# Kernel optimization log

Measured on AMD Instinct MI355X. Metric: run time of the kernel, lower is better.

The kernel has to match this reference:

```python
import jax, jax.numpy as jnp
import numpy as np

B, N, M = 32, 4096, 32
IN_F, OUT_F, A = 256, 256, 8


def setup_inputs() -> dict:
    key = jax.random.key(0)
    k1, k2, k3, k4, k5 = jax.random.split(key, 5)
    fatoms = jax.random.normal(k1, (B, N, IN_F), dtype=jnp.float32)
    agraph = jax.random.randint(k2, (B, N, M), 0, N, dtype=jnp.int64)
    anchor_indices = jax.random.randint(k3, (B, A), 0, N, dtype=jnp.int64)
    # xavier-uniform-like init for W and a
    wlim = float(np.sqrt(6.0 / (IN_F + OUT_F)))
    alim = float(np.sqrt(6.0 / (2 * OUT_F + 1)))
    W = jax.random.uniform(k4, (IN_F, OUT_F), dtype=jnp.float32, minval=-wlim, maxval=wlim)
    a = jax.random.uniform(k5, (2 * OUT_F, 1), dtype=jnp.float32, minval=-alim, maxval=alim)
    return {"fatoms": fatoms, "agraph": agraph, "anchor_indices": anchor_indices, "W": W, "a": a}


def reference(fatoms, agraph, anchor_indices, W, a):
    # h: (B, N, F)
    h = jnp.matmul(fatoms, W)
    F_ = h.shape[-1]
    # gather anchor features: (B, A, F)
    anchor_feat = jnp.take_along_axis(h, anchor_indices[:, :, None], axis=1)
    # e = cat([h_self + h_anch, h_self - h_anch]) @ a, decomposed to avoid the
    # (B, N, A, 2F) intermediate: e = h @ (a1+a2) + h_anch @ (a1-a2)
    a1 = a[:F_, 0]
    a2 = a[F_:, 0]
    e = (h @ (a1 + a2))[:, :, None] + (anchor_feat @ (a1 - a2))[:, None, :]  # (B, N, A)
    # mask[b,n,k] = anchor_indices[b,k] in agraph[b,n,:]  (vectorized torch.isin)
    mask = (agraph[:, :, None, :] == anchor_indices[:, None, :, None]).any(axis=-1)  # (B, N, A)
    e = jnp.where(mask, e, jnp.float32(-1e9))
    attn = jax.nn.softmax(e, axis=-1)
    # weighted sum of anchor features: (B, N, F)
    return jnp.einsum('bna,baf->bnf', attn, anchor_feat)
```

## Files before the change

### kernel.cpp

```cpp
#include <hip/hip_runtime.h>

#define B_ 32
#define N_ 4096
#define M_ 32
#define F_ 256
#define A_ 8

typedef float f32x4 __attribute__((ext_vector_type(4)));
typedef int   i32x4 __attribute__((ext_vector_type(4)));

#define WS_AF 0
#define WS_E2 (B_ * A_ * F_)

__global__ __launch_bounds__(256) void anchor_kernel(const float* __restrict__ fatoms,
                                                     const int* __restrict__ anchor_idx,
                                                     const float* __restrict__ W,
                                                     const float* __restrict__ a,
                                                     float* __restrict__ ws) {
    int bk = blockIdx.x;
    int b  = bk / A_;
    int f  = threadIdx.x;
    __shared__ float xs[F_];
    __shared__ float red[F_];
    int idx = anchor_idx[bk];
    xs[f] = fatoms[((size_t)b * N_ + idx) * F_ + f];
    __syncthreads();
    float acc[4] = {0.f, 0.f, 0.f, 0.f};
    for (int i0 = 0; i0 < F_; i0 += 16) {
#pragma unroll
        for (int j = 0; j < 16; ++j)
            acc[j & 3] += xs[i0 + j] * W[(i0 + j) * F_ + f];
    }
    float accs = (acc[0] + acc[1]) + (acc[2] + acc[3]);
    ws[WS_AF + bk * F_ + f] = accs;
    red[f] = accs * (a[f] - a[f + F_]);
    __syncthreads();
    for (int s = 128; s > 0; s >>= 1) {
        if (f < s) red[f] += red[f + s];
        __syncthreads();
    }
    if (f == 0) ws[WS_E2 + bk] = red[0];
}

#define RPW 64

__global__ __launch_bounds__(64) void main_kernel(const int* __restrict__ agraph,
                                                  const int* __restrict__ anchor_idx,
                                                  const float* __restrict__ ws,
                                                  float* __restrict__ out) {
    int lane = threadIdx.x;
    const int chunks_per_batch = N_ / RPW;
    int b     = blockIdx.x / chunks_per_batch;
    int chunk = blockIdx.x % chunks_per_batch;
    int row0  = chunk * RPW;

    const i32x4* gp = (const i32x4*)(agraph + ((size_t)b * N_ + row0 + lane) * M_);
    i32x4 g[M_ / 4];
#pragma unroll
    for (int j = 0; j < M_ / 4; ++j) g[j] = gp[j];

    const float* af = ws + WS_AF + b * (A_ * F_);
    const float* e2 = ws + WS_E2 + b * A_;

    __shared__ float attn[RPW][A_];

    int   anch[A_];
    float e2r[A_];
#pragma unroll
    for (int k = 0; k < A_; ++k) {
        anch[k] = anchor_idx[b * A_ + k];
        e2r[k]  = e2[k];
    }
    float m8 = e2r[0];
#pragma unroll
    for (int k = 1; k < A_; ++k) m8 = fmaxf(m8, e2r[k]);
    float E[A_];
#pragma unroll
    for (int k = 0; k < A_; ++k) E[k] = __expf(e2r[k] - m8);

    f32x4 afr[A_];
#pragma unroll
    for (int k = 0; k < A_; ++k) afr[k] = *(const f32x4*)(af + k * F_ + lane * 4);

    {
        unsigned mk = 0;
#pragma unroll
        for (int j = 0; j < M_ / 4; ++j) {
#pragma unroll
            for (int k = 0; k < A_; ++k) {
                int hit = (g[j].x == anch[k]) | (g[j].y == anch[k]) |
                          (g[j].z == anch[k]) | (g[j].w == anch[k]);
                mk |= hit ? (1u << k) : 0u;
            }
        }
        float p[A_], s = 0.f;
#pragma unroll
        for (int k = 0; k < A_; ++k) { p[k] = (mk & (1u << k)) ? E[k] : 0.f; s += p[k]; }
        if (mk == 0) {
#pragma unroll
            for (int k = 0; k < A_; ++k) p[k] = 1.f;
            s = 8.f;
        }
        float rinv = __builtin_amdgcn_rcpf(s);
#pragma unroll
        for (int k = 0; k < A_; ++k) attn[lane][k] = p[k] * rinv;
    }
    __syncthreads();

    size_t base = ((size_t)b * N_ + row0) * F_ + lane * 4;
    for (int r0 = 0; r0 < RPW; r0 += 4) {
        f32x4 o[4];
#pragma unroll
        for (int u = 0; u < 4; ++u) {
            f32x4 pa = *(const f32x4*)&attn[r0 + u][0];
            f32x4 pb = *(const f32x4*)&attn[r0 + u][4];
            f32x4 t = pa.x * afr[0];
            t += pa.y * afr[1];
            t += pa.z * afr[2];
            t += pa.w * afr[3];
            t += pb.x * afr[4];
            t += pb.y * afr[5];
            t += pb.z * afr[6];
            t += pb.w * afr[7];
            o[u] = t;
        }
#pragma unroll
        for (int u = 0; u < 4; ++u)
            *(f32x4*)(out + base + (size_t)(r0 + u) * F_) = o[u];
    }
}

extern "C" void kernel_launch(void* const* d_in, const int* in_sizes, int n_in,
                              void* d_out, int out_size, void* d_ws, size_t ws_size,
                              hipStream_t stream) {
    const float* fatoms     = (const float*)d_in[0];
    const int*   agraph     = (const int*)d_in[1];
    const int*   anchor_idx = (const int*)d_in[2];
    const float* W          = (const float*)d_in[3];
    const float* a          = (const float*)d_in[4];
    float*       out        = (float*)d_out;
    float*       ws         = (float*)d_ws;

    hipLaunchKernelGGL(anchor_kernel, dim3(B_ * A_), dim3(256), 0, stream,
                       fatoms, anchor_idx, W, a, ws);
    hipLaunchKernelGGL(main_kernel, dim3(B_ * (N_ / RPW)), dim3(64), 0, stream,
                       agraph, anchor_idx, ws, out);
}
```

Baseline: 37.32 us.

## Split fused kernel into separate attention and output-store kernels

Splits the fused mask/softmax/store kernel into two launches when workspace allows. The first computes the attention weights per row and writes them to workspace; the second reads them back and writes the weighted anchor sums. The intent is to separate the agraph-read phase from the output-write phase so each kernel streams one kind of traffic. The cost is an extra launch plus writing and re-reading a (B,N,8) attention buffer. The old fused kernel is kept as a fallback when the workspace is too small.

```diff
diff --git a/kernel.cpp b/kernel.cpp
--- a/kernel.cpp
+++ b/kernel.cpp
@@ -11,6 +11,8 @@
 
 #define WS_AF 0
 #define WS_E2 (B_ * A_ * F_)
+#define WS_ATTN (WS_E2 + B_ * A_)
+#define WS_FLOATS_NEEDED (WS_ATTN + B_ * N_ * A_)
 
 __global__ __launch_bounds__(256) void anchor_kernel(const float* __restrict__ fatoms,
                                                      const int* __restrict__ anchor_idx,
@@ -42,17 +44,108 @@
     if (f == 0) ws[WS_E2 + bk] = red[0];
 }
 
-#define RPW 64
-
-__global__ __launch_bounds__(64) void main_kernel(const int* __restrict__ agraph,
+__global__ __launch_bounds__(64) void attn_kernel(const int* __restrict__ agraph,
                                                   const int* __restrict__ anchor_idx,
                                                   const float* __restrict__ ws,
-                                                  float* __restrict__ out) {
+                                                  float* __restrict__ attn) {
+    int lane = threadIdx.x;
+    const int chunks_per_batch = N_ / 64;
+    int b    = blockIdx.x / chunks_per_batch;
+    int row  = (blockIdx.x % chunks_per_batch) * 64 + lane;
+
+    const i32x4* gp = (const i32x4*)(agraph + ((size_t)b * N_ + row) * M_);
+    i32x4 g[M_ / 4];
+#pragma unroll
+    for (int j = 0; j < M_ / 4; ++j) g[j] = gp[j];
+
+    int   anch[A_];
+    float e2r[A_];
+#pragma unroll
+    for (int k = 0; k < A_; ++k) {
+        anch[k] = anchor_idx[b * A_ + k];
+        e2r[k]  = ws[WS_E2 + b * A_ + k];
+    }
+    float m8 = e2r[0];
+#pragma unroll
+    for (int k = 1; k < A_; ++k) m8 = fmaxf(m8, e2r[k]);
+    float E[A_];
+#pragma unroll
+    for (int k = 0; k < A_; ++k) E[k] = __expf(e2r[k] - m8);
+
+    unsigned mk = 0;
+#pragma unroll
+    for (int j = 0; j < M_ / 4; ++j) {
+#pragma unroll
+        for (int k = 0; k < A_; ++k) {
+            int hit = (g[j].x == anch[k]) | (g[j].y == anch[k]) |
+                      (g[j].z == anch[k]) | (g[j].w == anch[k]);
+            mk |= hit ? (1u << k) : 0u;
+        }
+    }
+    float p[A_], s = 0.f;
+#pragma unroll
+    for (int k = 0; k < A_; ++k) { p[k] = (mk & (1u << k)) ? E[k] : 0.f; s += p[k]; }
+    if (mk == 0) {
+#pragma unroll
+        for (int k = 0; k < A_; ++k) p[k] = 1.f;
+        s = 8.f;
+    }
+    float rinv = __builtin_amdgcn_rcpf(s);
+    f32x4 pa = {p[0] * rinv, p[1] * rinv, p[2] * rinv, p[3] * rinv};
+    f32x4 pb = {p[4] * rinv, p[5] * rinv, p[6] * rinv, p[7] * rinv};
+    f32x4* ap = (f32x4*)(attn + ((size_t)b * N_ + row) * A_);
+    ap[0] = pa;
+    ap[1] = pb;
+}
+
+#define RPW 64
+
+__global__ __launch_bounds__(64) void store_kernel(const float* __restrict__ ws,
+                                                   const float* __restrict__ attn,
+                                                   float* __restrict__ out) {
     int lane = threadIdx.x;
     const int chunks_per_batch = N_ / RPW;
-    int b     = blockIdx.x / chunks_per_batch;
-    int chunk = blockIdx.x % chunks_per_batch;
-    int row0  = chunk * RPW;
+    int b    = blockIdx.x / chunks_per_batch;
+    int row0 = (blockIdx.x % chunks_per_batch) * RPW;
+
+    const float* af = ws + WS_AF + b * (A_ * F_);
+    f32x4 afr[A_];
+#pragma unroll
+    for (int k = 0; k < A_; ++k) afr[k] = *(const f32x4*)(af + k * F_ + lane * 4);
+
+    const float* ab = attn + ((size_t)b * N_ + row0) * A_;
+    size_t base = ((size_t)b * N_ + row0) * F_ + lane * 4;
+    for (int r0 = 0; r0 < RPW; r0 += 4) {
+        f32x4 o[4];
+#pragma unroll
+        for (int u = 0; u < 4; ++u) {
+            const float* pr = ab + (size_t)(r0 + u) * A_;
+            f32x4 pa = *(const f32x4*)pr;
+            f32x4 pb = *(const f32x4*)(pr + 4);
+            f32x4 t = pa.x * afr[0];
+            t += pa.y * afr[1];
+            t += pa.z * afr[2];
+            t += pa.w * afr[3];
+            t += pb.x * afr[4];
+            t += pb.y * afr[5];
+            t += pb.z * afr[6];
+            t += pb.w * afr[7];
+            o[u] = t;
+        }
+#pragma unroll
+        for (int u = 0; u < 4; ++u)
+            *(f32x4*)(out + base + (size_t)(r0 + u) * F_) = o[u];
+    }
+}
+
+__global__ __launch_bounds__(64) void fused_kernel(const int* __restrict__ agraph,
+                                                   const int* __restrict__ anchor_idx,
+                                                   const float* __restrict__ ws,
+                                                   float* __restrict__ out) {
+    int lane = threadIdx.x;
+    const int chunks_per_batch = N_ / RPW;
+    int b    = blockIdx.x / chunks_per_batch;
+    int row0 = (blockIdx.x % chunks_per_batch) * RPW;
 
     const i32x4* gp = (const i32x4*)(agraph + ((size_t)b * N_ + row0 + lane) * M_);
     i32x4 g[M_ / 4];
@@ -60,16 +153,13 @@
     for (int j = 0; j < M_ / 4; ++j) g[j] = gp[j];
 
     const float* af = ws + WS_AF + b * (A_ * F_);
-    const float* e2 = ws + WS_E2 + b * A_;
-
-    __shared__ float attn[RPW][A_];
-
+    __shared__ float attn_s[RPW][A_];
     int   anch[A_];
     float e2r[A_];
 #pragma unroll
     for (int k = 0; k < A_; ++k) {
         anch[k] = anchor_idx[b * A_ + k];
-        e2r[k]  = e2[k];
+        e2r[k]  = ws[WS_E2 + b * A_ + k];
     }
     float m8 = e2r[0];
 #pragma unroll
@@ -77,11 +167,9 @@
     float E[A_];
 #pragma unroll
     for (int k = 0; k < A_; ++k) E[k] = __expf(e2r[k] - m8);
-
     f32x4 afr[A_];
 #pragma unroll
     for (int k = 0; k < A_; ++k) afr[k] = *(const f32x4*)(af + k * F_ + lane * 4);
-
     {
         unsigned mk = 0;
 #pragma unroll
@@ -103,17 +191,16 @@
         }
         float rinv = __builtin_amdgcn_rcpf(s);
 #pragma unroll
-        for (int k = 0; k < A_; ++k) attn[lane][k] = p[k] * rinv;
+        for (int k = 0; k < A_; ++k) attn_s[lane][k] = p[k] * rinv;
     }
     __syncthreads();
-
     size_t base = ((size_t)b * N_ + row0) * F_ + lane * 4;
     for (int r0 = 0; r0 < RPW; r0 += 4) {
         f32x4 o[4];
 #pragma unroll
         for (int u = 0; u < 4; ++u) {
-            f32x4 pa = *(const f32x4*)&attn[r0 + u][0];
-            f32x4 pb = *(const f32x4*)&attn[r0 + u][4];
+            f32x4 pa = *(const f32x4*)&attn_s[r0 + u][0];
+            f32x4 pb = *(const f32x4*)&attn_s[r0 + u][4];
             f32x4 t = pa.x * afr[0];
             t += pa.y * afr[1];
             t += pa.z * afr[2];
@@ -143,6 +230,15 @@
 
     hipLaunchKernelGGL(anchor_kernel, dim3(B_ * A_), dim3(256), 0, stream,
                        fatoms, anchor_idx, W, a, ws);
-    hipLaunchKernelGGL(main_kernel, dim3(B_ * (N_ / RPW)), dim3(64), 0, stream,
-                       agraph, anchor_idx, ws, out);
-}
+
+    if (ws_size >= (size_t)WS_FLOATS_NEEDED * sizeof(float)) {
+        float* attn = ws + WS_ATTN;
+        hipLaunchKernelGGL(attn_kernel, dim3(B_ * (N_ / 64)), dim3(64), 0, stream,
+                           agraph, anchor_idx, ws, attn);
+        hipLaunchKernelGGL(store_kernel, dim3(B_ * (N_ / RPW)), dim3(64), 0, stream,
+                           ws, attn, out);
+    } else {
+        hipLaunchKernelGGL(fused_kernel, dim3(B_ * (N_ / RPW)), dim3(64), 0, stream,
+                           agraph, anchor_idx, ws, out);
+    }
+}
```

Measured after the change: 42.24 us. +13.2%, slower.
